# Kernel optimization log

Hardware: AMD Instinct MI355X
Metric: run time of the kernel (lower is better)

Reference implementation:

```python
import jax, jax.numpy as jnp
import numpy as np

HD, L, HEADS, C = 128, 4, 4, 32
EG = np.linspace(-3.0, 3.0, 100)


def _ln(x, s, b, eps=1e-5):
    mu = jnp.mean(x, -1, keepdims=True)
    var = jnp.mean((x - mu) ** 2, -1, keepdims=True)
    return (x - mu) / jnp.sqrt(var + eps) * s + b


def _gat(h, e, src, dst, W, asrc, adst, We, aedge, bias):
    # PyG GATConv (shared src/dst lin, edge_dim, add_self_loops with mean fill)
    N = h.shape[0]
    xl = (h @ W).reshape(N, HEADS, C)
    el = (e @ We).reshape(-1, HEADS, C)
    el_full = jnp.concatenate([el, jnp.broadcast_to(el.mean(0), (N, HEADS, C))], 0)
    ar = jnp.arange(N, dtype=src.dtype)
    sf = jnp.concatenate([src, ar])
    df = jnp.concatenate([dst, ar])
    alpha = (xl[sf] * asrc).sum(-1) + (xl[df] * adst).sum(-1) + (el_full * aedge).sum(-1)
    alpha = jnp.where(alpha > 0, alpha, 0.2 * alpha)  # leaky_relu(0.2)
    m = jax.ops.segment_max(alpha, df, num_segments=N)
    ex = jnp.exp(alpha - m[df])
    den = jax.ops.segment_sum(ex, df, num_segments=N)
    w = ex / den[df]
    out = jax.ops.segment_sum(xl[sf] * w[..., None], df, num_segments=N)
    return out.reshape(N, HEADS * C) + bias


def _forward(x, edge_index, edge_attr, batch, GammaL, GammaR, node_w, node_b,
             edgep_w, edgep_b, gat_lin, att_src, att_dst, gat_lin_edge, att_edge,
             gat_bias, ln_s, ln_b, on_w1, on_b1, on_w2, on_b2, cp_w1, cp_b1, cp_w2, cp_b2):
    src, dst = edge_index[0], edge_index[1]
    B, Hs = GammaL.shape
    h = x @ node_w + node_b
    e = edge_attr @ edgep_w + edgep_b
    for i in range(L):
        hc = _gat(h, e, src, dst, gat_lin[i], att_src[i], att_dst[i],
                  gat_lin_edge[i], att_edge[i], gat_bias[i])
        h = _ln(jax.nn.relu(hc) + h, ln_s[i], ln_b[i])
    # --- block Hamiltonian assembly (n_orb = 1) ---
    dna = jnp.any(x != 0, axis=1)          # contact nodes have all-zero features
    mi = dna.astype(jnp.int32)
    cexc = jnp.cumsum(mi) - mi             # exclusive dna rank over all nodes
    per = jax.ops.segment_sum(mi, batch, num_segments=B)
    before = jnp.cumsum(per) - per
    local = cexc - before[batch]           # local dna index within each graph
    onsite = (jax.nn.relu(h @ on_w1 + on_b1) @ on_w2 + on_b2)[:, 0]
    coup = (jax.nn.relu(e @ cp_w1 + cp_b1) @ cp_w2 + cp_b2)[:, 0]
    H = jnp.zeros((B, Hs, Hs), jnp.float32)
    H = H.at[batch, local, local].add(jnp.where(dna, onsite, 0.0))
    em = dna[src] & dna[dst]               # edges fully inside the DNA block
    u, v, be = local[src], local[dst], batch[src]
    cv = jnp.where(em, coup, 0.0)
    H = H.at[be, u, v].add(cv)
    H = H.at[be, v, u].add(cv)             # hermitian (scalar block)
    I = jnp.eye(Hs, dtype=jnp.float32)
    H = H + 1e-6 * I
    # --- NEGF, Frobenius (real-arithmetic) formulation ---
    Eg = jnp.asarray(EG, jnp.float32)
    A = Eg[None, :, None, None] * I - H[:, None]           # [B,E,Hs,Hs]
    gamma = GammaL + GammaR
    Bm = 0.5 * gamma[:, None, :, None] * I + 1e-12 * I     # [B,1,Hs,Hs] diag
    A_inv = jnp.linalg.inv(A)
    Gr_real = jnp.linalg.inv(A + Bm @ A_inv @ Bm)
    Gr_imag = -(A_inv @ Bm) @ Gr_real
    dos = jnp.log10(jnp.maximum(-jnp.einsum('benn->be', Gr_imag) / np.pi, 1e-16))
    G2 = Gr_real ** 2 + Gr_imag ** 2
    T = jnp.einsum('bi,beij,bj->be', GammaL, G2, GammaR)   # Tr(GL G GR Gd)
    T = jnp.log10(jnp.maximum(T, 1e-16))
    return T, dos, H


def setup_inputs() -> dict:
    key = jax.random.key(0)
    ks = jax.random.split(key, 32)
    B, n_dna, n_con = 8, 128, 2
    n_per = n_dna + n_con
    N = B * n_per
    srcs, dsts = [], []
    for g in range(B):
        base = g * n_per
        for i in range(n_con, n_per - 1):
            srcs.append(base + i); dsts.append(base + i + 1)
        for i in range(n_con, n_per - 2):
            srcs.append(base + i); dsts.append(base + i + 2)
        srcs += [base, base + 1]
        dsts += [base + n_con, base + n_per - 1]
    edge_index = jnp.asarray(np.stack([srcs, dsts]), dtype=jnp.int32)
    E = edge_index.shape[1]
    batch = jnp.asarray(np.repeat(np.arange(B), n_per), dtype=jnp.int32)
    contact = np.zeros(N, bool)
    for g in range(B):
        contact[g * n_per] = True
        contact[g * n_per + 1] = True
    x = jax.random.normal(ks[0], (N, 4), jnp.float32) * jnp.asarray(~contact, jnp.float32)[:, None]
    edge_attr = jax.random.normal(ks[1], (E, 5), jnp.float32)
    GammaL = jax.random.uniform(ks[2], (B, n_dna), jnp.float32) * 0.1
    GammaR = jax.random.uniform(ks[3], (B, n_dna), jnp.float32) * 0.1
    p = lambda k, s: jax.random.normal(k, s, jnp.float32) * 0.05
    hd = HD
    return dict(
        x=x, edge_index=edge_index, edge_attr=edge_attr, batch=batch,
        GammaL=GammaL, GammaR=GammaR,
        node_w=p(ks[4], (4, hd)), node_b=jnp.zeros(hd),
        edgep_w=p(ks[5], (5, hd)), edgep_b=jnp.zeros(hd),
        gat_lin=p(ks[6], (L, hd, hd)), att_src=p(ks[7], (L, HEADS, C)),
        att_dst=p(ks[8], (L, HEADS, C)), gat_lin_edge=p(ks[9], (L, hd, hd)),
        att_edge=p(ks[10], (L, HEADS, C)), gat_bias=jnp.zeros((L, hd)),
        ln_s=jnp.ones((L, hd)), ln_b=jnp.zeros((L, hd)),
        on_w1=p(ks[11], (hd, hd // 2)), on_b1=jnp.zeros(hd // 2),
        on_w2=p(ks[12], (hd // 2, 1)), on_b2=jnp.zeros(1),
        cp_w1=p(ks[13], (hd, hd // 2)), cp_b1=jnp.zeros(hd // 2),
        cp_w2=p(ks[14], (hd // 2, 1)), cp_b2=jnp.zeros(1))


def reference(x, edge_index, edge_attr, batch, GammaL, GammaR, node_w, node_b,
              edgep_w, edgep_b, gat_lin, att_src, att_dst, gat_lin_edge, att_edge,
              gat_bias, ln_s, ln_b, on_w1, on_b1, on_w2, on_b2, cp_w1, cp_b1, cp_w2, cp_b2):
    return _forward(x, edge_index, edge_attr, batch, GammaL, GammaR, node_w, node_b,
                    edgep_w, edgep_b, gat_lin, att_src, att_dst, gat_lin_edge, att_edge,
                    gat_bias, ln_s, ln_b, on_w1, on_b1, on_w2, on_b2, cp_w1, cp_b1, cp_w2, cp_b2)
```

## Files before the change

### kernel.cpp

```cpp
#include <hip/hip_runtime.h>

#define HSZ 128
#define NEGRID 100

typedef float v2f __attribute__((ext_vector_type(2)));

__global__ void k_embed(const float* __restrict__ x, const float* __restrict__ ea,
                        const float* __restrict__ nw, const float* __restrict__ nb,
                        const float* __restrict__ ew, const float* __restrict__ eb,
                        float* __restrict__ h, float* __restrict__ e,
                        float* __restrict__ smean, int* __restrict__ cnt,
                        int N, int E) {
  int row = blockIdx.x, c = threadIdx.x;
  if (row == 0 && c < 16) smean[c] = 0.f;
  if (row < N) {
    if (c == 0) cnt[row] = 0;
    float acc = nb[c];
#pragma unroll
    for (int k = 0; k < 4; ++k) acc += x[row * 4 + k] * nw[k * 128 + c];
    h[row * 128 + c] = acc;
  } else {
    int ei = row - N;
    float acc = eb[c];
#pragma unroll
    for (int k = 0; k < 5; ++k) acc += ea[ei * 5 + k] * ew[k * 128 + c];
    e[ei * 128 + c] = acc;
  }
}

__global__ void k_csr(const int* __restrict__ dstI, int* __restrict__ cnt,
                      int* __restrict__ csr, int E) {
  int e = blockIdx.x * 256 + threadIdx.x;
  if (e >= E) return;
  int d = dstI[e];
  int j = atomicAdd(&cnt[d], 1);
  if (j < 4) csr[d * 4 + j] = e;
}

__global__ void k_edge(const float* __restrict__ e, const float* __restrict__ gat_lin_edge,
                       const float* __restrict__ att_edge, float* __restrict__ sedge,
                       float* __restrict__ smean, int E) {
  __shared__ float row_lds[128];
  __shared__ float red[128];
  int gid = blockIdx.x, c = threadIdx.x;
  int l = gid / E, ei = gid - l * E;
  row_lds[c] = e[ei * 128 + c];
  __syncthreads();
  const float* We = gat_lin_edge + (size_t)l * 16384;
  float acc = 0.f;
  for (int k = 0; k < 128; ++k) acc += row_lds[k] * We[k * 128 + c];
  red[c] = acc * att_edge[l * 128 + c];
  __syncthreads();
  if (c < 4) {
    float s = 0.f;
    for (int t = 0; t < 32; ++t) s += red[c * 32 + t];
    sedge[(size_t)l * E * 4 + ei * 4 + c] = s;
    atomicAdd(&smean[l * 4 + c], s);
  }
}

__global__ void k_gat_lin(const float* __restrict__ h, const float* __restrict__ W,
                          const float* __restrict__ asrc, const float* __restrict__ adst,
                          float* __restrict__ xl, float* __restrict__ ssrc,
                          float* __restrict__ sdst, int N) {
  __shared__ float row_lds[128];
  __shared__ float red[128];
  __shared__ float red2[128];
  int row = blockIdx.x, c = threadIdx.x;
  row_lds[c] = h[row * 128 + c];
  __syncthreads();
  float acc = 0.f;
  for (int k = 0; k < 128; ++k) acc += row_lds[k] * W[k * 128 + c];
  xl[row * 128 + c] = acc;
  red[c]  = acc * asrc[c];
  red2[c] = acc * adst[c];
  __syncthreads();
  if (c < 8) {
    int hh = c & 3;
    const float* b = (c < 4) ? red : red2;
    float s = 0.f;
    for (int t = 0; t < 32; ++t) s += b[hh * 32 + t];
    if (c < 4) ssrc[row * 4 + hh] = s; else sdst[row * 4 + hh] = s;
  }
}

__global__ void k_gather(const float* __restrict__ ssrc, const float* __restrict__ sdst,
                         const float* __restrict__ sedge, const float* __restrict__ smean4,
                         const float* __restrict__ xl, const int* __restrict__ srcI,
                         const int* __restrict__ cnt, const int* __restrict__ csr,
                         const float* __restrict__ bias, const float* __restrict__ lns,
                         const float* __restrict__ lnb, float* __restrict__ h,
                         int N, float invE) {
  __shared__ float als[5][4];
  __shared__ float wts[5][4];
  __shared__ int sidx[5];
  __shared__ float buf[128];
  int n = blockIdx.x, c = threadIdx.x, hh = c >> 5;
  int deg = cnt[n];
  if (c < (deg + 1) * 4) {
    int j = c >> 2, h4 = c & 3;
    float a;
    if (j < deg) {
      int e = csr[n * 4 + j];
      int s = srcI[e];
      if (h4 == 0) sidx[j] = s;
      a = ssrc[s * 4 + h4] + sdst[n * 4 + h4] + sedge[e * 4 + h4];
    } else {
      if (h4 == 0) sidx[j] = n;
      a = ssrc[n * 4 + h4] + sdst[n * 4 + h4] + smean4[h4] * invE;
    }
    a = (a > 0.f) ? a : 0.2f * a;
    als[j][h4] = a;
  }
  __syncthreads();
  if (c < 4) {
    float m = -1e30f;
    for (int j = 0; j <= deg; ++j) m = fmaxf(m, als[j][c]);
    float den = 0.f;
    for (int j = 0; j <= deg; ++j) den += expf(als[j][c] - m);
    float id = 1.f / den;
    for (int j = 0; j <= deg; ++j) wts[j][c] = expf(als[j][c] - m) * id;
  }
  __syncthreads();
  float out = 0.f;
  for (int j = 0; j <= deg; ++j)
    out += wts[j][hh] * xl[sidx[j] * 128 + c];
  float v = fmaxf(out + bias[c], 0.f) + h[n * 128 + c];
  buf[c] = v;
  __syncthreads();
  for (int s = 64; s > 0; s >>= 1) { if (c < s) buf[c] += buf[c + s]; __syncthreads(); }
  float mean = buf[0] * (1.f / 128.f);
  __syncthreads();
  float dv = v - mean;
  buf[c] = dv * dv;
  __syncthreads();
  for (int s = 64; s > 0; s >>= 1) { if (c < s) buf[c] += buf[c + s]; __syncthreads(); }
  float var = buf[0] * (1.f / 128.f);
  h[n * 128 + c] = dv * (1.0f / sqrtf(var + 1e-5f)) * lns[c] + lnb[c];
}

__global__ void k_mlp(const float* __restrict__ h, const float* __restrict__ e,
                      const float* __restrict__ w1n, const float* __restrict__ b1n,
                      const float* __restrict__ w2n, const float* __restrict__ b2n,
                      const float* __restrict__ w1e, const float* __restrict__ b1e,
                      const float* __restrict__ w2e, const float* __restrict__ b2e,
                      float* __restrict__ onsite, float* __restrict__ coup, int N, int E) {
  int row = blockIdx.x, t = threadIdx.x;
  const float *vec, *w1, *b1, *w2; float b2v;
  if (row < N) { vec = h + (size_t)row * 128; w1 = w1n; b1 = b1n; w2 = w2n; b2v = b2n[0]; }
  else         { vec = e + (size_t)(row - N) * 128; w1 = w1e; b1 = b1e; w2 = w2e; b2v = b2e[0]; }
  float acc = b1[t];
  for (int k = 0; k < 128; ++k) acc += vec[k] * w1[k * 64 + t];
  acc = fmaxf(acc, 0.f) * w2[t];
#pragma unroll
  for (int off = 32; off; off >>= 1) acc += __shfl_down(acc, off);
  if (t == 0) {
    float r = acc + b2v;
    if (row < N) onsite[row] = r; else coup[row - N] = r;
  }
}

__global__ void k_dna(const float* __restrict__ x, const int* __restrict__ batch,
                      int* __restrict__ dna, int* __restrict__ loc, int N, int B) {
  __shared__ int perB[64];
  __shared__ int beforeB[64];
  int l = threadIdx.x;
  perB[l] = 0;
  __syncthreads();
  int chunk = (N + 63) >> 6;
  int s0 = l * chunk, s1 = min(N, s0 + chunk);
  int cnt = 0;
  for (int n = s0; n < s1; ++n) {
    int mi = (x[n * 4 + 0] != 0.f || x[n * 4 + 1] != 0.f ||
              x[n * 4 + 2] != 0.f || x[n * 4 + 3] != 0.f) ? 1 : 0;
    dna[n] = mi;
    cnt += mi;
    if (mi) atomicAdd(&perB[batch[n]], 1);
  }
  __syncthreads();
  int pre = cnt;
#pragma unroll
  for (int off = 1; off < 64; off <<= 1) {
    int o = __shfl_up(pre, off);
    if (l >= off) pre += o;
  }
  int excl = pre - cnt;
  if (l == 0) {
    int run = 0;
    for (int g = 0; g < B; ++g) { beforeB[g] = run; run += perB[g]; }
  }
  __syncthreads();
  int run = excl;
  for (int n = s0; n < s1; ++n) {
    loc[n] = run - beforeB[batch[n]];
    run += dna[n];
  }
}

__global__ void k_hbuild(const int* __restrict__ dna, const int* __restrict__ loc,
                         const int* __restrict__ batch, const int* __restrict__ srcI,
                         const int* __restrict__ dstI, const float* __restrict__ onsite,
                         const float* __restrict__ coup, float* __restrict__ H,
                         int N, int E) {
  int g = blockIdx.x, t = threadIdx.x;
  float* Hg = H + (size_t)g * HSZ * HSZ;
  for (int i = t; i < HSZ * HSZ; i += 256)
    Hg[i] = ((i >> 7) == (i & 127)) ? 1e-6f : 0.f;
  __syncthreads();
  for (int n = t; n < N; n += 256)
    if (batch[n] == g && dna[n]) Hg[loc[n] * (HSZ + 1)] += onsite[n];
  for (int e = t; e < E; e += 256) {
    int s = srcI[e], d = dstI[e];
    if (batch[s] == g && dna[s] && dna[d]) {
      float cv = coup[e];
      Hg[loc[s] * HSZ + loc[d]] += cv;
      Hg[loc[d] * HSZ + loc[s]] += cv;
    }
  }
}

__global__ __attribute__((amdgpu_flat_work_group_size(1024, 1024), amdgpu_waves_per_eu(8, 8)))
void k_negf(
    const float* __restrict__ Hm, const float* __restrict__ GL, const float* __restrict__ GR,
    float* __restrict__ outT, float* __restrict__ outD) {
  int bid = blockIdx.x;
  int b = bid / NEGRID, eix = bid % NEGRID;
  float Ev = (float)(-3.0 + (6.0 / 99.0) * (double)eix);

  int tid = threadIdx.x;
  int w = tid >> 6, l = tid & 63;
  int c0 = w << 3, r0 = l << 1;

  __shared__ float gl_s[HSZ], gr_s[HSZ], g_s[HSZ];
  __shared__ v2f fcol[2][HSZ];
  __shared__ v2f prow[16 * 8];
  __shared__ float redbuf[32];

  if (tid < HSZ) {
    float a_ = GL[b * HSZ + tid], b_ = GR[b * HSZ + tid];
    gl_s[tid] = a_; gr_s[tid] = b_;
    g_s[tid] = 0.5f * (a_ + b_) + 1e-12f;
  }
  __syncthreads();

  v2f z00, z01, z02, z03, z04, z05, z06, z07;
  v2f z10, z11, z12, z13, z14, z15, z16, z17;
  const float* Hb = Hm + (size_t)b * HSZ * HSZ;
#define INITR(Z0, Z1, Z2, Z3, Z4, Z5, Z6, Z7, RR) do { \
    int r_ = r0 + RR; \
    const float4 hA = *(const float4*)(Hb + r_ * HSZ + c0); \
    const float4 hB = *(const float4*)(Hb + r_ * HSZ + c0 + 4); \
    float gv = g_s[r_]; \
    Z0 = (v2f){((c0 + 0 == r_) ? Ev : 0.f) - hA.x, (c0 + 0 == r_) ? gv : 0.f}; \
    Z1 = (v2f){((c0 + 1 == r_) ? Ev : 0.f) - hA.y, (c0 + 1 == r_) ? gv : 0.f}; \
    Z2 = (v2f){((c0 + 2 == r_) ? Ev : 0.f) - hA.z, (c0 + 2 == r_) ? gv : 0.f}; \
    Z3 = (v2f){((c0 + 3 == r_) ? Ev : 0.f) - hA.w, (c0 + 3 == r_) ? gv : 0.f}; \
    Z4 = (v2f){((c0 + 4 == r_) ? Ev : 0.f) - hB.x, (c0 + 4 == r_) ? gv : 0.f}; \
    Z5 = (v2f){((c0 + 5 == r_) ? Ev : 0.f) - hB.y, (c0 + 5 == r_) ? gv : 0.f}; \
    Z6 = (v2f){((c0 + 6 == r_) ? Ev : 0.f) - hB.z, (c0 + 6 == r_) ? gv : 0.f}; \
    Z7 = (v2f){((c0 + 7 == r_) ? Ev : 0.f) - hB.w, (c0 + 7 == r_) ? gv : 0.f}; \
  } while (0)
  INITR(z00, z01, z02, z03, z04, z05, z06, z07, 0);
  INITR(z10, z11, z12, z13, z14, z15, z16, z17, 1);

  if (w == 0) { fcol[0][r0] = z00; fcol[0][r0 + 1] = z10; }
  if (l == 0) {
    v2f* pw = &prow[w << 3];
    pw[0] = z00; pw[1] = z01; pw[2] = z02; pw[3] = z03;
    pw[4] = z04; pw[5] = z05; pw[6] = z06; pw[7] = z07;
    if (w == 0) pw[0] = (v2f){z00.x + 1.f, z00.y};
  }
  __syncthreads();

  for (int k = 0; k < HSZ; ++k) {
    int par = k & 1, par2 = par ^ 1;
    v2f pv = fcol[par][k];
    float dmag = pv.x * pv.x + pv.y * pv.y;
    float idn = __builtin_amdgcn_rcpf(dmag);
    idn = idn * (2.0f - dmag * idn);
    float dre = pv.x * idn, dim = -pv.y * idn;

    v2f f0 = fcol[par][r0], f1 = fcol[par][r0 + 1];
    float f0x = f0.x - ((r0 == k) ? 1.f : 0.f);
    float f1x = f1.x - ((r0 + 1 == k) ? 1.f : 0.f);
    float fr0 = f0x * dre - f0.y * dim, fi0 = f0x * dim + f0.y * dre;
    float fr1 = f1x * dre - f1.y * dim, fi1 = f1x * dim + f1.y * dre;
    v2f ar0 = (v2f){-fr0, -fr0}, br0 = (v2f){fi0, -fi0};
    v2f ar1 = (v2f){-fr1, -fr1}, br1 = (v2f){fi1, -fi1};

    const v2f* qp = &prow[w << 3];
#define CELP(Z, AR, BR, Q, QS) do { \
      Z = __builtin_elementwise_fma(AR, Q, Z); \
      Z = __builtin_elementwise_fma(BR, QS, Z); \
    } while (0)
    {
      v2f q0 = qp[0], q1 = qp[1], q2 = qp[2], q3 = qp[3];
      v2f s0 = __builtin_shufflevector(q0, q0, 1, 0);
      v2f s1 = __builtin_shufflevector(q1, q1, 1, 0);
      v2f s2 = __builtin_shufflevector(q2, q2, 1, 0);
      v2f s3 = __builtin_shufflevector(q3, q3, 1, 0);
      CELP(z00, ar0, br0, q0, s0); CELP(z01, ar0, br0, q1, s1);
      CELP(z02, ar0, br0, q2, s2); CELP(z03, ar0, br0, q3, s3);
      CELP(z10, ar1, br1, q0, s0); CELP(z11, ar1, br1, q1, s1);
      CELP(z12, ar1, br1, q2, s2); CELP(z13, ar1, br1, q3, s3);
    }
    {
      v2f q4 = qp[4], q5 = qp[5], q6 = qp[6], q7 = qp[7];
      v2f s4 = __builtin_shufflevector(q4, q4, 1, 0);
      v2f s5 = __builtin_shufflevector(q5, q5, 1, 0);
      v2f s6 = __builtin_shufflevector(q6, q6, 1, 0);
      v2f s7 = __builtin_shufflevector(q7, q7, 1, 0);
      CELP(z04, ar0, br0, q4, s4); CELP(z05, ar0, br0, q5, s5);
      CELP(z06, ar0, br0, q6, s6); CELP(z07, ar0, br0, q7, s7);
      CELP(z14, ar1, br1, q4, s4); CELP(z15, ar1, br1, q5, s5);
      CELP(z16, ar1, br1, q6, s6); CELP(z17, ar1, br1, q7, s7);
    }

    int kn = k + 1;
    if (kn < HSZ) {
      bool stgw = (w == (kn >> 3));
      v2f v0 = (v2f){0.f, 0.f}, v1 = v0;
      if (stgw) {
        switch (kn & 7) {
          case 0:  v0 = z00; v1 = z10; break;
          case 1:  v0 = z01; v1 = z11; break;
          case 2:  v0 = z02; v1 = z12; break;
          case 3:  v0 = z03; v1 = z13; break;
          case 4:  v0 = z04; v1 = z14; break;
          case 5:  v0 = z05; v1 = z15; break;
          case 6:  v0 = z06; v1 = z16; break;
          default: v0 = z07; v1 = z17; break;
        }
        fcol[par2][r0] = v0;
        fcol[par2][r0 + 1] = v1;
      }
      bool myl = (l == (kn >> 1));
      v2f* pw = &prow[w << 3];
      if ((kn & 1) == 0) {
        if (myl) {
          pw[0] = z00; pw[1] = z01; pw[2] = z02; pw[3] = z03;
          pw[4] = z04; pw[5] = z05; pw[6] = z06; pw[7] = z07;
        }
      } else {
        if (myl) {
          pw[0] = z10; pw[1] = z11; pw[2] = z12; pw[3] = z13;
          pw[4] = z14; pw[5] = z15; pw[6] = z16; pw[7] = z17;
        }
      }
      if (stgw && myl) {
        v2f t = (kn & 1) ? v1 : v0;
        prow[(w << 3) + (kn & 7)] = (v2f){t.x + 1.f, t.y};
      }
    }
    __syncthreads();
  }

  float gw0 = gr_s[c0 + 0], gw1 = gr_s[c0 + 1], gw2 = gr_s[c0 + 2], gw3 = gr_s[c0 + 3];
  float gw4 = gr_s[c0 + 4], gw5 = gr_s[c0 + 5], gw6 = gr_s[c0 + 6], gw7 = gr_s[c0 + 7];
  float Tacc = 0.f, Dacc = 0.f;
#define ACCR(Z0, Z1, Z2, Z3, Z4, Z5, Z6, Z7, RR) do { \
    int rr_ = r0 + RR; \
    float glv = gl_s[rr_]; \
    float g2; \
    g2 = Z0.x * Z0.x + Z0.y * Z0.y; Tacc += glv * gw0 * g2; if (rr_ == c0 + 0) Dacc += Z0.y; \
    g2 = Z1.x * Z1.x + Z1.y * Z1.y; Tacc += glv * gw1 * g2; if (rr_ == c0 + 1) Dacc += Z1.y; \
    g2 = Z2.x * Z2.x + Z2.y * Z2.y; Tacc += glv * gw2 * g2; if (rr_ == c0 + 2) Dacc += Z2.y; \
    g2 = Z3.x * Z3.x + Z3.y * Z3.y; Tacc += glv * gw3 * g2; if (rr_ == c0 + 3) Dacc += Z3.y; \
    g2 = Z4.x * Z4.x + Z4.y * Z4.y; Tacc += glv * gw4 * g2; if (rr_ == c0 + 4) Dacc += Z4.y; \
    g2 = Z5.x * Z5.x + Z5.y * Z5.y; Tacc += glv * gw5 * g2; if (rr_ == c0 + 5) Dacc += Z5.y; \
    g2 = Z6.x * Z6.x + Z6.y * Z6.y; Tacc += glv * gw6 * g2; if (rr_ == c0 + 6) Dacc += Z6.y; \
    g2 = Z7.x * Z7.x + Z7.y * Z7.y; Tacc += glv * gw7 * g2; if (rr_ == c0 + 7) Dacc += Z7.y; \
  } while (0)
  ACCR(z00, z01, z02, z03, z04, z05, z06, z07, 0);
  ACCR(z10, z11, z12, z13, z14, z15, z16, z17, 1);
#pragma unroll
  for (int off = 32; off; off >>= 1) {
    Tacc += __shfl_xor(Tacc, off);
    Dacc += __shfl_xor(Dacc, off);
  }
  if (l == 0) { redbuf[w] = Tacc; redbuf[16 + w] = Dacc; }
  __syncthreads();
  if (tid == 0) {
    float T = 0.f, D = 0.f;
    for (int v = 0; v < 16; ++v) { T += redbuf[v]; D += redbuf[16 + v]; }
    outT[bid] = log10f(fmaxf(T, 1e-16f));
    outD[bid] = log10f(fmaxf(-D * 0.31830988618379067f, 1e-16f));
  }
}

extern "C" void kernel_launch(void* const* d_in, const int* in_sizes, int n_in,
                              void* d_out, int out_size, void* d_ws, size_t ws_size,
                              hipStream_t stream) {
  const float* x     = (const float*)d_in[0];
  const int*   eidx  = (const int*)d_in[1];
  const float* eattr = (const float*)d_in[2];
  const int*   batch = (const int*)d_in[3];
  const float* GL    = (const float*)d_in[4];
  const float* GR    = (const float*)d_in[5];
  const float* node_w  = (const float*)d_in[6];
  const float* node_b  = (const float*)d_in[7];
  const float* edgep_w = (const float*)d_in[8];
  const float* edgep_b = (const float*)d_in[9];
  const float* gat_lin      = (const float*)d_in[10];
  const float* att_src      = (const float*)d_in[11];
  const float* att_dst      = (const float*)d_in[12];
  const float* gat_lin_edge = (const float*)d_in[13];
  const float* att_edge     = (const float*)d_in[14];
  const float* gat_bias     = (const float*)d_in[15];
  const float* ln_s = (const float*)d_in[16];
  const float* ln_b = (const float*)d_in[17];
  const float* on_w1 = (const float*)d_in[18];
  const float* on_b1 = (const float*)d_in[19];
  const float* on_w2 = (const float*)d_in[20];
  const float* on_b2 = (const float*)d_in[21];
  const float* cp_w1 = (const float*)d_in[22];
  const float* cp_b1 = (const float*)d_in[23];
  const float* cp_w2 = (const float*)d_in[24];
  const float* cp_b2 = (const float*)d_in[25];

  int N = in_sizes[0] / 4;
  int E = in_sizes[1] / 2;
  int B = in_sizes[4] / HSZ;
  const int* srcI = eidx;
  const int* dstI = eidx + E;

  float* ws = (float*)d_ws;
  size_t o = 0;
  float* h     = ws + o; o += (size_t)N * 128;
  float* ebuf  = ws + o; o += (size_t)E * 128;
  float* xl    = ws + o; o += (size_t)N * 128;
  float* ssrc  = ws + o; o += (size_t)N * 4;
  float* sdst  = ws + o; o += (size_t)N * 4;
  float* sedge = ws + o; o += (size_t)E * 16;
  float* smean = ws + o; o += 16;
  float* onsite = ws + o; o += (size_t)((N + 3) & ~3);
  float* coup   = ws + o; o += (size_t)((E + 3) & ~3);
  int* dna = (int*)(ws + o); o += (size_t)((N + 3) & ~3);
  int* loc = (int*)(ws + o); o += (size_t)((N + 3) & ~3);
  int* cnt = (int*)(ws + o); o += (size_t)((N + 3) & ~3);
  int* csr = (int*)(ws + o); o += (size_t)N * 4;

  float* out  = (float*)d_out;
  float* outT = out;
  float* outD = out + (size_t)B * NEGRID;
  float* outH = out + (size_t)2 * B * NEGRID;

  k_embed<<<N + E, 128, 0, stream>>>(x, eattr, node_w, node_b, edgep_w, edgep_b,
                                     h, ebuf, smean, cnt, N, E);
  k_csr<<<(E + 255) / 256, 256, 0, stream>>>(dstI, cnt, csr, E);
  k_edge<<<4 * E, 128, 0, stream>>>(ebuf, gat_lin_edge, att_edge, sedge, smean, E);
  for (int l = 0; l < 4; ++l) {
    k_gat_lin<<<N, 128, 0, stream>>>(
        h, gat_lin + (size_t)l * 16384, att_src + l * 128, att_dst + l * 128,
        xl, ssrc, sdst, N);
    k_gather<<<N, 128, 0, stream>>>(
        ssrc, sdst, sedge + (size_t)l * E * 4, smean + l * 4, xl, srcI, cnt, csr,
        gat_bias + l * 128, ln_s + l * 128, ln_b + l * 128, h, N, 1.0f / (float)E);
  }
  k_mlp<<<N + E, 64, 0, stream>>>(h, ebuf, on_w1, on_b1, on_w2, on_b2,
                                  cp_w1, cp_b1, cp_w2, cp_b2, onsite, coup, N, E);
  k_dna<<<1, 64, 0, stream>>>(x, batch, dna, loc, N, B);
  k_hbuild<<<B, 256, 0, stream>>>(dna, loc, batch, srcI, dstI, onsite, coup,
                                  outH, N, E);
  k_negf<<<B * NEGRID, 1024, 0, stream>>>(outH, GL, GR, outT, outD);
}
```

Baseline: 651.1 us.

## Fuse pre-NEGF GNN stages into one cooperative persistent kernel

```diff
diff --git a/kernel.cpp b/kernel.cpp
--- a/kernel.cpp
+++ b/kernel.cpp
@@ -1,220 +1,229 @@
 #include <hip/hip_runtime.h>
+#include <hip/hip_cooperative_groups.h>
+
+namespace cg = cooperative_groups;
 
 #define HSZ 128
 #define NEGRID 100
 
 typedef float v2f __attribute__((ext_vector_type(2)));
 
-__global__ void k_embed(const float* __restrict__ x, const float* __restrict__ ea,
-                        const float* __restrict__ nw, const float* __restrict__ nb,
-                        const float* __restrict__ ew, const float* __restrict__ eb,
-                        float* __restrict__ h, float* __restrict__ e,
-                        float* __restrict__ smean, int* __restrict__ cnt,
-                        int N, int E) {
-  int row = blockIdx.x, c = threadIdx.x;
-  if (row == 0 && c < 16) smean[c] = 0.f;
-  if (row < N) {
-    if (c == 0) cnt[row] = 0;
-    float acc = nb[c];
-#pragma unroll
-    for (int k = 0; k < 4; ++k) acc += x[row * 4 + k] * nw[k * 128 + c];
-    h[row * 128 + c] = acc;
-  } else {
-    int ei = row - N;
-    float acc = eb[c];
-#pragma unroll
-    for (int k = 0; k < 5; ++k) acc += ea[ei * 5 + k] * ew[k * 128 + c];
-    e[ei * 128 + c] = acc;
-  }
-}
-
-__global__ void k_csr(const int* __restrict__ dstI, int* __restrict__ cnt,
-                      int* __restrict__ csr, int E) {
-  int e = blockIdx.x * 256 + threadIdx.x;
-  if (e >= E) return;
-  int d = dstI[e];
-  int j = atomicAdd(&cnt[d], 1);
-  if (j < 4) csr[d * 4 + j] = e;
-}
-
-__global__ void k_edge(const float* __restrict__ e, const float* __restrict__ gat_lin_edge,
-                       const float* __restrict__ att_edge, float* __restrict__ sedge,
-                       float* __restrict__ smean, int E) {
-  __shared__ float row_lds[128];
-  __shared__ float red[128];
-  int gid = blockIdx.x, c = threadIdx.x;
-  int l = gid / E, ei = gid - l * E;
-  row_lds[c] = e[ei * 128 + c];
-  __syncthreads();
-  const float* We = gat_lin_edge + (size_t)l * 16384;
-  float acc = 0.f;
-  for (int k = 0; k < 128; ++k) acc += row_lds[k] * We[k * 128 + c];
-  red[c] = acc * att_edge[l * 128 + c];
-  __syncthreads();
-  if (c < 4) {
-    float s = 0.f;
-    for (int t = 0; t < 32; ++t) s += red[c * 32 + t];
-    sedge[(size_t)l * E * 4 + ei * 4 + c] = s;
-    atomicAdd(&smean[l * 4 + c], s);
-  }
-}
-
-__global__ void k_gat_lin(const float* __restrict__ h, const float* __restrict__ W,
-                          const float* __restrict__ asrc, const float* __restrict__ adst,
-                          float* __restrict__ xl, float* __restrict__ ssrc,
-                          float* __restrict__ sdst, int N) {
-  __shared__ float row_lds[128];
-  __shared__ float red[128];
-  __shared__ float red2[128];
-  int row = blockIdx.x, c = threadIdx.x;
-  row_lds[c] = h[row * 128 + c];
-  __syncthreads();
-  float acc = 0.f;
-  for (int k = 0; k < 128; ++k) acc += row_lds[k] * W[k * 128 + c];
-  xl[row * 128 + c] = acc;
-  red[c]  = acc * asrc[c];
-  red2[c] = acc * adst[c];
-  __syncthreads();
-  if (c < 8) {
-    int hh = c & 3;
-    const float* b = (c < 4) ? red : red2;
-    float s = 0.f;
-    for (int t = 0; t < 32; ++t) s += b[hh * 32 + t];
-    if (c < 4) ssrc[row * 4 + hh] = s; else sdst[row * 4 + hh] = s;
-  }
-}
-
-__global__ void k_gather(const float* __restrict__ ssrc, const float* __restrict__ sdst,
-                         const float* __restrict__ sedge, const float* __restrict__ smean4,
-                         const float* __restrict__ xl, const int* __restrict__ srcI,
-                         const int* __restrict__ cnt, const int* __restrict__ csr,
-                         const float* __restrict__ bias, const float* __restrict__ lns,
-                         const float* __restrict__ lnb, float* __restrict__ h,
-                         int N, float invE) {
-  __shared__ float als[5][4];
-  __shared__ float wts[5][4];
+struct MegaArgs {
+  const float *x, *ea; const int *eidx, *batch;
+  const float *nw, *nb, *ew, *eb;
+  const float *glin, *asrc_a, *adst_a, *gline, *aedge_a, *gbias, *lns_a, *lnb_a;
+  const float *on_w1, *on_b1, *on_w2, *on_b2, *cp_w1, *cp_b1, *cp_w2, *cp_b2;
+  float *h, *ebuf, *xl, *ssrc, *sdst, *sedge, *smean, *onsite, *coup;
+  int *dna, *loc, *cnt, *csr; float *H;
+  int N, E, B;
+};
+
+__global__ void k_mega(MegaArgs a) {
+  cg::grid_group grid = cg::this_grid();
+  const int bid = blockIdx.x, c = threadIdx.x, G = gridDim.x;
+  const int N = a.N, E = a.E, B = a.B;
+  const int* srcI = a.eidx;
+  const int* dstI = a.eidx + E;
+  __shared__ float row_lds[128], red[128], red2[128];
+  __shared__ float als[5][4], wts[5][4];
   __shared__ int sidx[5];
   __shared__ float buf[128];
-  int n = blockIdx.x, c = threadIdx.x, hh = c >> 5;
-  int deg = cnt[n];
-  if (c < (deg + 1) * 4) {
-    int j = c >> 2, h4 = c & 3;
-    float a;
-    if (j < deg) {
-      int e = csr[n * 4 + j];
-      int s = srcI[e];
-      if (h4 == 0) sidx[j] = s;
-      a = ssrc[s * 4 + h4] + sdst[n * 4 + h4] + sedge[e * 4 + h4];
+  __shared__ int perB[64], beforeB[64];
+
+  if (bid == 0 && c < 16) a.smean[c] = 0.f;
+  for (int row = bid; row < N + E; row += G) {
+    if (row < N) {
+      if (c == 0) a.cnt[row] = 0;
+      float acc = a.nb[c];
+#pragma unroll
+      for (int k = 0; k < 4; ++k) acc += a.x[row * 4 + k] * a.nw[k * 128 + c];
+      a.h[row * 128 + c] = acc;
     } else {
-      if (h4 == 0) sidx[j] = n;
-      a = ssrc[n * 4 + h4] + sdst[n * 4 + h4] + smean4[h4] * invE;
-    }
-    a = (a > 0.f) ? a : 0.2f * a;
-    als[j][h4] = a;
-  }
-  __syncthreads();
-  if (c < 4) {
-    float m = -1e30f;
-    for (int j = 0; j <= deg; ++j) m = fmaxf(m, als[j][c]);
-    float den = 0.f;
-    for (int j = 0; j <= deg; ++j) den += expf(als[j][c] - m);
-    float id = 1.f / den;
-    for (int j = 0; j <= deg; ++j) wts[j][c] = expf(als[j][c] - m) * id;
-  }
-  __syncthreads();
-  float out = 0.f;
-  for (int j = 0; j <= deg; ++j)
-    out += wts[j][hh] * xl[sidx[j] * 128 + c];
-  float v = fmaxf(out + bias[c], 0.f) + h[n * 128 + c];
-  buf[c] = v;
-  __syncthreads();
-  for (int s = 64; s > 0; s >>= 1) { if (c < s) buf[c] += buf[c + s]; __syncthreads(); }
-  float mean = buf[0] * (1.f / 128.f);
-  __syncthreads();
-  float dv = v - mean;
-  buf[c] = dv * dv;
-  __syncthreads();
-  for (int s = 64; s > 0; s >>= 1) { if (c < s) buf[c] += buf[c + s]; __syncthreads(); }
-  float var = buf[0] * (1.f / 128.f);
-  h[n * 128 + c] = dv * (1.0f / sqrtf(var + 1e-5f)) * lns[c] + lnb[c];
-}
-
-__global__ void k_mlp(const float* __restrict__ h, const float* __restrict__ e,
-                      const float* __restrict__ w1n, const float* __restrict__ b1n,
-                      const float* __restrict__ w2n, const float* __restrict__ b2n,
-                      const float* __restrict__ w1e, const float* __restrict__ b1e,
-                      const float* __restrict__ w2e, const float* __restrict__ b2e,
-                      float* __restrict__ onsite, float* __restrict__ coup, int N, int E) {
-  int row = blockIdx.x, t = threadIdx.x;
-  const float *vec, *w1, *b1, *w2; float b2v;
-  if (row < N) { vec = h + (size_t)row * 128; w1 = w1n; b1 = b1n; w2 = w2n; b2v = b2n[0]; }
-  else         { vec = e + (size_t)(row - N) * 128; w1 = w1e; b1 = b1e; w2 = w2e; b2v = b2e[0]; }
-  float acc = b1[t];
-  for (int k = 0; k < 128; ++k) acc += vec[k] * w1[k * 64 + t];
-  acc = fmaxf(acc, 0.f) * w2[t];
+      int ei = row - N;
+      float acc = a.eb[c];
 #pragma unroll
-  for (int off = 32; off; off >>= 1) acc += __shfl_down(acc, off);
-  if (t == 0) {
-    float r = acc + b2v;
-    if (row < N) onsite[row] = r; else coup[row - N] = r;
-  }
-}
-
-__global__ void k_dna(const float* __restrict__ x, const int* __restrict__ batch,
-                      int* __restrict__ dna, int* __restrict__ loc, int N, int B) {
-  __shared__ int perB[64];
-  __shared__ int beforeB[64];
-  int l = threadIdx.x;
-  perB[l] = 0;
-  __syncthreads();
-  int chunk = (N + 63) >> 6;
-  int s0 = l * chunk, s1 = min(N, s0 + chunk);
-  int cnt = 0;
-  for (int n = s0; n < s1; ++n) {
-    int mi = (x[n * 4 + 0] != 0.f || x[n * 4 + 1] != 0.f ||
-              x[n * 4 + 2] != 0.f || x[n * 4 + 3] != 0.f) ? 1 : 0;
-    dna[n] = mi;
-    cnt += mi;
-    if (mi) atomicAdd(&perB[batch[n]], 1);
-  }
-  __syncthreads();
-  int pre = cnt;
+      for (int k = 0; k < 5; ++k) acc += a.ea[ei * 5 + k] * a.ew[k * 128 + c];
+      a.ebuf[ei * 128 + c] = acc;
+    }
+  }
+  grid.sync();
+
+  for (int e = bid * 128 + c; e < E; e += G * 128) {
+    int d = dstI[e];
+    int j = atomicAdd(&a.cnt[d], 1);
+    if (j < 4) a.csr[d * 4 + j] = e;
+  }
+  for (int item = bid; item < 4 * E; item += G) {
+    int l = item / E, ei = item - l * E;
+    row_lds[c] = a.ebuf[ei * 128 + c];
+    __syncthreads();
+    const float* We = a.gline + (size_t)l * 16384;
+    float acc = 0.f;
+    for (int k = 0; k < 128; ++k) acc += row_lds[k] * We[k * 128 + c];
+    red[c] = acc * a.aedge_a[l * 128 + c];
+    __syncthreads();
+    if (c < 4) {
+      float s = 0.f;
+      for (int t = 0; t < 32; ++t) s += red[c * 32 + t];
+      a.sedge[(size_t)l * E * 4 + ei * 4 + c] = s;
+      atomicAdd(&a.smean[l * 4 + c], s);
+    }
+    __syncthreads();
+  }
+  grid.sync();
+
+  for (int l = 0; l < 4; ++l) {
+    const float* W = a.glin + (size_t)l * 16384;
+    const float* asrc = a.asrc_a + l * 128;
+    const float* adst = a.adst_a + l * 128;
+    for (int row = bid; row < N; row += G) {
+      row_lds[c] = a.h[row * 128 + c];
+      __syncthreads();
+      float acc = 0.f;
+      for (int k = 0; k < 128; ++k) acc += row_lds[k] * W[k * 128 + c];
+      a.xl[row * 128 + c] = acc;
+      red[c]  = acc * asrc[c];
+      red2[c] = acc * adst[c];
+      __syncthreads();
+      if (c < 8) {
+        int hh = c & 3;
+        const float* b = (c < 4) ? red : red2;
+        float s = 0.f;
+        for (int t = 0; t < 32; ++t) s += b[hh * 32 + t];
+        if (c < 4) a.ssrc[row * 4 + hh] = s; else a.sdst[row * 4 + hh] = s;
+      }
+      __syncthreads();
+    }
+    grid.sync();
+
+    const float* sedge_l = a.sedge + (size_t)l * E * 4;
+    const float* smean4 = a.smean + l * 4;
+    const float* bias = a.gbias + l * 128;
+    const float* lns = a.lns_a + l * 128;
+    const float* lnb = a.lnb_a + l * 128;
+    float invE = 1.0f / (float)E;
+    for (int n = bid; n < N; n += G) {
+      int hh = c >> 5;
+      int deg = a.cnt[n];
+      if (c < (deg + 1) * 4) {
+        int j = c >> 2, h4 = c & 3;
+        float al;
+        if (j < deg) {
+          int e = a.csr[n * 4 + j];
+          int s = srcI[e];
+          if (h4 == 0) sidx[j] = s;
+          al = a.ssrc[s * 4 + h4] + a.sdst[n * 4 + h4] + sedge_l[e * 4 + h4];
+        } else {
+          if (h4 == 0) sidx[j] = n;
+          al = a.ssrc[n * 4 + h4] + a.sdst[n * 4 + h4] + smean4[h4] * invE;
+        }
+        al = (al > 0.f) ? al : 0.2f * al;
+        als[j][h4] = al;
+      }
+      __syncthreads();
+      if (c < 4) {
+        float m = -1e30f;
+        for (int j = 0; j <= deg; ++j) m = fmaxf(m, als[j][c]);
+        float den = 0.f;
+        for (int j = 0; j <= deg; ++j) den += expf(als[j][c] - m);
+        float id = 1.f / den;
+        for (int j = 0; j <= deg; ++j) wts[j][c] = expf(als[j][c] - m) * id;
+      }
+      __syncthreads();
+      float out = 0.f;
+      for (int j = 0; j <= deg; ++j)
+        out += wts[j][hh] * a.xl[sidx[j] * 128 + c];
+      float v = fmaxf(out + bias[c], 0.f) + a.h[n * 128 + c];
+      buf[c] = v;
+      __syncthreads();
+      for (int s = 64; s > 0; s >>= 1) { if (c < s) buf[c] += buf[c + s]; __syncthreads(); }
+      float mean = buf[0] * (1.f / 128.f);
+      __syncthreads();
+      float dv = v - mean;
+      buf[c] = dv * dv;
+      __syncthreads();
+      for (int s = 64; s > 0; s >>= 1) { if (c < s) buf[c] += buf[c + s]; __syncthreads(); }
+      float var = buf[0] * (1.f / 128.f);
+      a.h[n * 128 + c] = dv * (1.0f / sqrtf(var + 1e-5f)) * lns[c] + lnb[c];
+      __syncthreads();
+    }
+    grid.sync();
+  }
+
+  if (bid != G - 1) {
+    int wv = c >> 6, t = c & 63;
+    for (int base = 2 * bid; base < N + E; base += 2 * (G - 1)) {
+      int row = base + wv;
+      if (row < N + E) {
+        const float *vec, *w1, *b1, *w2; float b2v;
+        if (row < N) { vec = a.h + (size_t)row * 128; w1 = a.on_w1; b1 = a.on_b1; w2 = a.on_w2; b2v = a.on_b2[0]; }
+        else         { vec = a.ebuf + (size_t)(row - N) * 128; w1 = a.cp_w1; b1 = a.cp_b1; w2 = a.cp_w2; b2v = a.cp_b2[0]; }
+        float acc = b1[t];
+        for (int k = 0; k < 128; ++k) acc += vec[k] * w1[k * 64 + t];
+        acc = fmaxf(acc, 0.f) * w2[t];
 #pragma unroll
-  for (int off = 1; off < 64; off <<= 1) {
-    int o = __shfl_up(pre, off);
-    if (l >= off) pre += o;
-  }
-  int excl = pre - cnt;
-  if (l == 0) {
-    int run = 0;
-    for (int g = 0; g < B; ++g) { beforeB[g] = run; run += perB[g]; }
-  }
-  __syncthreads();
-  int run = excl;
-  for (int n = s0; n < s1; ++n) {
-    loc[n] = run - beforeB[batch[n]];
-    run += dna[n];
-  }
-}
-
-__global__ void k_hbuild(const int* __restrict__ dna, const int* __restrict__ loc,
-                         const int* __restrict__ batch, const int* __restrict__ srcI,
-                         const int* __restrict__ dstI, const float* __restrict__ onsite,
-                         const float* __restrict__ coup, float* __restrict__ H,
-                         int N, int E) {
-  int g = blockIdx.x, t = threadIdx.x;
-  float* Hg = H + (size_t)g * HSZ * HSZ;
-  for (int i = t; i < HSZ * HSZ; i += 256)
-    Hg[i] = ((i >> 7) == (i & 127)) ? 1e-6f : 0.f;
-  __syncthreads();
-  for (int n = t; n < N; n += 256)
-    if (batch[n] == g && dna[n]) Hg[loc[n] * (HSZ + 1)] += onsite[n];
-  for (int e = t; e < E; e += 256) {
-    int s = srcI[e], d = dstI[e];
-    if (batch[s] == g && dna[s] && dna[d]) {
-      float cv = coup[e];
-      Hg[loc[s] * HSZ + loc[d]] += cv;
-      Hg[loc[d] * HSZ + loc[s]] += cv;
+        for (int off = 32; off; off >>= 1) acc += __shfl_down(acc, off);
+        if (t == 0) {
+          float r = acc + b2v;
+          if (row < N) a.onsite[row] = r; else a.coup[row - N] = r;
+        }
+      }
+    }
+  } else {
+    if (c < 64) perB[c] = 0;
+    __syncthreads();
+    int chunk = (N + 63) >> 6;
+    int cnt_ = 0;
+    if (c < 64) {
+      int s0 = c * chunk, s1 = min(N, s0 + chunk);
+      for (int n = s0; n < s1; ++n) {
+        int mi = (a.x[n * 4 + 0] != 0.f || a.x[n * 4 + 1] != 0.f ||
+                  a.x[n * 4 + 2] != 0.f || a.x[n * 4 + 3] != 0.f) ? 1 : 0;
+        a.dna[n] = mi;
+        cnt_ += mi;
+        if (mi) atomicAdd(&perB[a.batch[n]], 1);
+      }
+    }
+    __syncthreads();
+    if (c < 64) {
+      int pre = cnt_;
+#pragma unroll
+      for (int off = 1; off < 64; off <<= 1) {
+        int o = __shfl_up(pre, off);
+        if (c >= off) pre += o;
+      }
+      int excl = pre - cnt_;
+      if (c == 0) {
+        int run = 0;
+        for (int g = 0; g < B; ++g) { beforeB[g] = run; run += perB[g]; }
+      }
+      __syncthreads();
+      int run = excl;
+      int s0 = c * chunk, s1 = min(N, s0 + chunk);
+      for (int n = s0; n < s1; ++n) {
+        a.loc[n] = run - beforeB[a.batch[n]];
+        run += a.dna[n];
+      }
+    } else {
+      __syncthreads();
+    }
+  }
+  grid.sync();
+
+  if (bid < B) {
+    float* Hg = a.H + (size_t)bid * HSZ * HSZ;
+    for (int i = c; i < HSZ * HSZ; i += 128)
+      Hg[i] = ((i >> 7) == (i & 127)) ? 1e-6f : 0.f;
+    __syncthreads();
+    for (int n = c; n < N; n += 128)
+      if (a.batch[n] == bid && a.dna[n]) Hg[a.loc[n] * (HSZ + 1)] += a.onsite[n];
+    for (int e = c; e < E; e += 128) {
+      int s = srcI[e], d = dstI[e];
+      if (a.batch[s] == bid && a.dna[s] && a.dna[d]) {
+        float cv = a.coup[e];
+        Hg[a.loc[s] * HSZ + a.loc[d]] += cv;
+        Hg[a.loc[d] * HSZ + a.loc[s]] += cv;
+      }
     }
   }
 }
@@ -421,8 +430,6 @@
   int N = in_sizes[0] / 4;
   int E = in_sizes[1] / 2;
   int B = in_sizes[4] / HSZ;
-  const int* srcI = eidx;
-  const int* dstI = eidx + E;
 
   float* ws = (float*)d_ws;
   size_t o = 0;
@@ -445,22 +452,20 @@
   float* outD = out + (size_t)B * NEGRID;
   float* outH = out + (size_t)2 * B * NEGRID;
 
-  k_embed<<<N + E, 128, 0, stream>>>(x, eattr, node_w, node_b, edgep_w, edgep_b,
-                                     h, ebuf, smean, cnt, N, E);
-  k_csr<<<(E + 255) / 256, 256, 0, stream>>>(dstI, cnt, csr, E);
-  k_edge<<<4 * E, 128, 0, stream>>>(ebuf, gat_lin_edge, att_edge, sedge, smean, E);
-  for (int l = 0; l < 4; ++l) {
-    k_gat_lin<<<N, 128, 0, stream>>>(
-        h, gat_lin + (size_t)l * 16384, att_src + l * 128, att_dst + l * 128,
-        xl, ssrc, sdst, N);
-    k_gather<<<N, 128, 0, stream>>>(
-        ssrc, sdst, sedge + (size_t)l * E * 4, smean + l * 4, xl, srcI, cnt, csr,
-        gat_bias + l * 128, ln_s + l * 128, ln_b + l * 128, h, N, 1.0f / (float)E);
-  }
-  k_mlp<<<N + E, 64, 0, stream>>>(h, ebuf, on_w1, on_b1, on_w2, on_b2,
-                                  cp_w1, cp_b1, cp_w2, cp_b2, onsite, coup, N, E);
-  k_dna<<<1, 64, 0, stream>>>(x, batch, dna, loc, N, B);
-  k_hbuild<<<B, 256, 0, stream>>>(dna, loc, batch, srcI, dstI, onsite, coup,
-                                  outH, N, E);
+  MegaArgs ma;
+  ma.x = x; ma.ea = eattr; ma.eidx = eidx; ma.batch = batch;
+  ma.nw = node_w; ma.nb = node_b; ma.ew = edgep_w; ma.eb = edgep_b;
+  ma.glin = gat_lin; ma.asrc_a = att_src; ma.adst_a = att_dst;
+  ma.gline = gat_lin_edge; ma.aedge_a = att_edge; ma.gbias = gat_bias;
+  ma.lns_a = ln_s; ma.lnb_a = ln_b;
+  ma.on_w1 = on_w1; ma.on_b1 = on_b1; ma.on_w2 = on_w2; ma.on_b2 = on_b2;
+  ma.cp_w1 = cp_w1; ma.cp_b1 = cp_b1; ma.cp_w2 = cp_w2; ma.cp_b2 = cp_b2;
+  ma.h = h; ma.ebuf = ebuf; ma.xl = xl; ma.ssrc = ssrc; ma.sdst = sdst;
+  ma.sedge = sedge; ma.smean = smean; ma.onsite = onsite; ma.coup = coup;
+  ma.dna = dna; ma.loc = loc; ma.cnt = cnt; ma.csr = csr; ma.H = outH;
+  ma.N = N; ma.E = E; ma.B = B;
+
+  void* kargs[] = { (void*)&ma };
+  hipLaunchCooperativeKernel((const void*)k_mega, dim3(N), dim3(128), kargs, 0, stream);
   k_negf<<<B * NEGRID, 1024, 0, stream>>>(outH, GL, GR, outT, outD);
 }
```

Result: slower. 1.848 ms (+183.9%).
